# Performance work log

Measured on AMD Instinct MI355X. Metric: run time of the kernel, lower is better.

The kernel has to match this reference:

```python
import jax, jax.numpy as jnp
import numpy as np

BILATERAL = True
THETA_ALPHA = 8.0   # spatial bandwidth for bilateral term
THETA_BETA = 0.5    # color bandwidth for bilateral term
THETA_GAMMA = 3.0   # spatial bandwidth for spatial-only term


def _features(input_image):
    # input_image: [B, Ci, H, W] -> features [B, N, D]
    B, Ci, H, W = input_image.shape
    N = H * W
    ys, xs = jnp.meshgrid(jnp.arange(H, dtype=jnp.float32),
                          jnp.arange(W, dtype=jnp.float32), indexing='ij')
    pos = jnp.stack([ys, xs], axis=-1).reshape(N, 2)  # [N, 2]
    if BILATERAL:
        sp = jnp.broadcast_to(pos / THETA_ALPHA, (B, N, 2))
        col = input_image.reshape(B, Ci, N).transpose(0, 2, 1) / THETA_BETA  # [B, N, Ci]
        return jnp.concatenate([sp, col], axis=-1)  # [B, N, 2+Ci]
    else:
        return jnp.broadcast_to(pos / THETA_GAMMA, (B, N, 2))


def _gauss_filter(values, feats):
    # values: [B, C, N]; feats: [B, N, D] -> [B, C, N]
    # K_ij = exp(-0.5 * ||f_i - f_j||^2) (unnormalized, as in permutohedral filtering)
    sq = jnp.sum(feats * feats, axis=-1)  # [B, N]
    # squared distances: [B, N, N]
    d2 = sq[:, :, None] + sq[:, None, :] - 2.0 * jnp.einsum('bnd,bmd->bnm', feats, feats)
    K = jnp.exp(-0.5 * jnp.maximum(d2, 0.0))
    return jnp.einsum('bnm,bcm->bcn', K, values)


def setup_inputs() -> dict:
    key = jax.random.key(0)
    k1, k2 = jax.random.split(key)
    cur_state = jax.random.normal(k1, (2, 21, 96, 96), dtype=jnp.float32)
    input_image = jax.random.uniform(k2, (2, 3, 96, 96), dtype=jnp.float32)
    return {"cur_state": cur_state, "input_image": input_image}


def reference(cur_state, input_image):
    assert cur_state.ndim == 4
    B, C, H, W = cur_state.shape
    N = H * W
    feats = _features(input_image)                 # [B, N, D]
    vals = cur_state.reshape(B, C, N)              # [B, C, N]
    out = _gauss_filter(vals, feats)               # [B, C, N]
    return out.reshape(B, C, H, W)
```

## Files before the change

kernel.cpp:

```cpp
#include <hip/hip_runtime.h>
#include <hip/hip_bf16.h>
#include <math.h>


#define HH 96
#define WW 96
#define NN (HH * WW)
#define NB 2
#define NC 21

typedef __attribute__((ext_vector_type(8))) short short8;
typedef __attribute__((ext_vector_type(16))) float f32x16;

constexpr float INV_TA = 0.125f;
constexpr float INV_TB = 2.0f;
constexpr float LOG2E  = 1.44269504088896340736f;

constexpr int BLK   = 256;
constexpr int ITILE = 128;
constexpr int NIT   = NN / ITILE;
constexpr int NJB   = NN / 32;
constexpr int G     = 24;
constexpr int QW    = NJB / G;

constexpr size_t VG_BYTES = (size_t)NB * NJB * 128 * 16;
constexpr size_t FJA_OFF  = VG_BYTES;

constexpr int NVU = NB * NJB * 128;
constexpr int NFT = NB * NN;
constexpr int NZ  = NB * NC * NN / 4;
constexpr int PREP_TASKS = NVU + NFT + NZ;

#if defined(__has_builtin)
#if __has_builtin(__builtin_amdgcn_exp2f)
#define EXP2F(x) __builtin_amdgcn_exp2f(x)
#endif
#endif
#ifndef EXP2F
#define EXP2F(x) exp2f(x)
#endif

__device__ __forceinline__ unsigned short bf16_rne(float f) {
    __hip_bfloat16 h = __float2bfloat16(f);
    unsigned short u; __builtin_memcpy(&u, &h, 2); return u;
}
__device__ __forceinline__ float bf16_f(unsigned short u) {
    __hip_bfloat16 h; __builtin_memcpy(&h, &u, 2); return __bfloat162float(h);
}
__device__ __forceinline__ unsigned pk2(float a, float b) {
    const unsigned u0 = __float_as_uint(a) + 0x8000u;
    const unsigned u1 = __float_as_uint(b) + 0x8000u;
    return __builtin_amdgcn_perm(u1, u0, 0x07060302u);
}

__global__ __launch_bounds__(BLK)
void prep_kernel(const float* __restrict__ cur, const float* __restrict__ img,
                 unsigned char* __restrict__ ws, float* __restrict__ out) {
    const int t = blockIdx.x * BLK + threadIdx.x;
    if (t < NVU) {
        const int c    = t & 31;
        const int h    = (t >> 5) & 1;
        const int m    = (t >> 6) & 1;
        const int jw   = t >> 7;
        const int b    = jw / NJB;
        const int jblk = jw % NJB;
        const int jb = jblk * 32 + m * 16 + 4 * h;
        float4 qa = {0, 0, 0, 0}, qb = {0, 0, 0, 0};
        if (c < NC) {
            const float* row = cur + ((size_t)b * NC + c) * NN;
            qa = *(const float4*)(row + jb);
            qb = *(const float4*)(row + jb + 8);
        }
        uint4 o;
        o.x = pk2(qa.x, qa.y); o.y = pk2(qa.z, qa.w);
        o.z = pk2(qb.x, qb.y); o.w = pk2(qb.z, qb.w);
        *(uint4*)(ws + (size_t)t * 16) = o;
    } else if (t < NVU + NFT) {
        const int tf = t - NVU;
        const int b = tf / NN;
        const int j = tf % NN;
        const float y = (float)(j / WW) * INV_TA;
        const float x = (float)(j % WW) * INV_TA;
        const float* ib = img + (size_t)b * 3 * NN;
        unsigned short ch[3], cl[3]; float cf[3];
        #pragma unroll
        for (int d = 0; d < 3; ++d) {
            const float c = ib[d * NN + j] * INV_TB;
            ch[d] = bf16_rne(c);
            const float chf = bf16_f(ch[d]);
            cl[d] = bf16_rne(c - chf);
            cf[d] = chf + bf16_f(cl[d]);
        }
        const float e = -0.5f * (y * y + x * x +
                                 cf[0] * cf[0] + cf[1] * cf[1] + cf[2] * cf[2]);
        const unsigned short eh = bf16_rne(e);
        const unsigned short el = bf16_rne(e - bf16_f(eh));
        const unsigned short yb = bf16_rne(y), xb = bf16_rne(x);
        const unsigned short one = 0x3F80;
        unsigned short* u0 = (unsigned short*)
            (ws + FJA_OFF + ((size_t)(b * 2 + 0) * NN + j) * 16);
        unsigned short* u1 = (unsigned short*)
            (ws + FJA_OFF + ((size_t)(b * 2 + 1) * NN + j) * 16);
        u0[0] = yb; u0[1] = xb; u0[2] = ch[0]; u0[3] = ch[1]; u0[4] = ch[2];
        u0[5] = cl[0]; u0[6] = cl[1]; u0[7] = cl[2];
        u1[0] = ch[0]; u1[1] = ch[1]; u1[2] = ch[2]; u1[3] = eh; u1[4] = el;
        u1[5] = one; u1[6] = one; u1[7] = 0;
    } else {
        ((float4*)out)[t - NVU - NFT] = float4{0.0f, 0.0f, 0.0f, 0.0f};
    }
}

__global__ __launch_bounds__(BLK)
void perm_gauss_mfma(const float* __restrict__ img,
                     const unsigned char* __restrict__ ws,
                     float* __restrict__ out) {
    __shared__ __align__(16) float tile[4 * 32 * 33];
    const int tid  = threadIdx.x;
    const int lane = tid & 63;
    const int wave = tid >> 6;
    const int il   = lane & 31;
    const int half = lane >> 5;

    const int it = blockIdx.x, g = blockIdx.y, b = blockIdx.z;
    const int ibase = it * ITILE + wave * 32;
    const float* imgb = img + (size_t)b * 3 * NN;
    float* outb = out + (size_t)b * NC * NN;

    const int ig = ibase + il;
    const float y = (float)(ig / WW) * INV_TA;
    const float x = (float)(ig % WW) * INV_TA;
    unsigned short ch[3], cl[3]; float cf[3];
    #pragma unroll
    for (int d = 0; d < 3; ++d) {
        const float c = imgb[d * NN + ig] * INV_TB;
        ch[d] = bf16_rne(c);
        const float chf = bf16_f(ch[d]);
        cl[d] = bf16_rne(c - chf);
        cf[d] = chf + bf16_f(cl[d]);
    }
    const float e = -0.5f * (y * y + x * x +
                             cf[0] * cf[0] + cf[1] * cf[1] + cf[2] * cf[2]);
    const unsigned short eh = bf16_rne(e);
    const unsigned short el = bf16_rne(e - bf16_f(eh));
    const unsigned short one = 0x3F80;
    union { unsigned short u[8]; short8 v; } bfi;
    if (half == 0) {
        bfi.u[0] = bf16_rne(y); bfi.u[1] = bf16_rne(x);
        bfi.u[2] = ch[0]; bfi.u[3] = ch[1]; bfi.u[4] = ch[2];
        bfi.u[5] = ch[0]; bfi.u[6] = ch[1]; bfi.u[7] = ch[2];
    } else {
        bfi.u[0] = cl[0]; bfi.u[1] = cl[1]; bfi.u[2] = cl[2];
        bfi.u[3] = one; bfi.u[4] = one; bfi.u[5] = eh; bfi.u[6] = el;
        bfi.u[7] = 0;
    }

    f32x16 acc, zz;
    #pragma unroll
    for (int r = 0; r < 16; ++r) { acc[r] = 0.0f; zz[r] = 0.0f; }

    const int jb0 = g * QW;
    const unsigned char* fp = ws + FJA_OFF +
        ((size_t)(b * 2 + half) * NN + (size_t)jb0 * 32 + il) * 16;
    const unsigned char* vp = ws +
        ((size_t)(b * NJB + jb0) * 128 + half * 32 + il) * 16;

    auto consume = [&](const f32x16& s, short8 V1, short8 V2) {
        float w[16];
        #pragma unroll
        for (int r = 0; r < 16; ++r) w[r] = EXP2F(s[r] * LOG2E);
        union { unsigned dw[4]; short8 v; } a1, a2;
        #pragma unroll
        for (int d = 0; d < 4; ++d) {
            a1.dw[d] = pk2(w[2 * d],     w[2 * d + 1]);
            a2.dw[d] = pk2(w[8 + 2 * d], w[9 + 2 * d]);
        }
        acc = __builtin_amdgcn_mfma_f32_32x32x16_bf16(a1.v, V1, acc, 0, 0, 0);
        acc = __builtin_amdgcn_mfma_f32_32x32x16_bf16(a2.v, V2, acc, 0, 0, 0);
    };

    short8 af0 = *(const short8*)fp;
    short8 af1 = *(const short8*)(fp + 512);
    short8 v1  = *(const short8*)vp;
    short8 v2  = *(const short8*)(vp + 1024);
    f32x16 s_cur = __builtin_amdgcn_mfma_f32_32x32x16_bf16(af0, bfi.v, zz, 0, 0, 0);

    #pragma unroll 2
    for (int q = 0; q < QW - 1; ++q) {
        const f32x16 s_next =
            __builtin_amdgcn_mfma_f32_32x32x16_bf16(af1, bfi.v, zz, 0, 0, 0);
        if (q < QW - 2) af1 = *(const short8*)(fp + 1024);
        fp += 512;
        const short8 v1n = *(const short8*)(vp + 2048);
        const short8 v2n = *(const short8*)(vp + 2048 + 1024);
        vp += 2048;
        consume(s_cur, v1, v2);
        s_cur = s_next; v1 = v1n; v2 = v2n;
    }
    consume(s_cur, v1, v2);

    float* mytile = tile + wave * (32 * 33);
    #pragma unroll
    for (int r = 0; r < 16; ++r) {
        const int row = (r & 3) + 8 * (r >> 2) + 4 * half;
        mytile[row * 33 + il] = acc[r];
    }
    #pragma unroll
    for (int cc = 0; cc < 11; ++cc) {
        const int c = 2 * cc + half;
        if (c < NC) {
            const float v = mytile[il * 33 + c];
            atomicAdd(&outb[(size_t)c * NN + ibase + il], v);
        }
    }
}

extern "C" void kernel_launch(void* const* d_in, const int* in_sizes, int n_in,
                              void* d_out, int out_size, void* d_ws, size_t ws_size,
                              hipStream_t stream) {
    const float* cur = (const float*)d_in[0];
    const float* img = (const float*)d_in[1];
    float* out = (float*)d_out;
    unsigned char* ws = (unsigned char*)d_ws;

    prep_kernel<<<PREP_TASKS / BLK, BLK, 0, stream>>>(cur, img, ws, out);
    dim3 grid(NIT, G, NB);
    perm_gauss_mfma<<<grid, BLK, 0, stream>>>(img, ws, out);
}
```

Baseline: 93.94 us.

## Split j-range across waves with in-block reduction before atomics

```diff
diff --git a/kernel.cpp b/kernel.cpp
--- a/kernel.cpp
+++ b/kernel.cpp
@@ -17,11 +17,11 @@
 constexpr float LOG2E  = 1.44269504088896340736f;
 
 constexpr int BLK   = 256;
-constexpr int ITILE = 128;
+constexpr int ITILE = 32;
 constexpr int NIT   = NN / ITILE;
 constexpr int NJB   = NN / 32;
-constexpr int G     = 24;
-constexpr int QW    = NJB / G;
+constexpr int G2    = 6;
+constexpr int QW    = NJB / (G2*4);
 
 constexpr size_t VG_BYTES = (size_t)NB * NJB * 128 * 16;
 constexpr size_t FJA_OFF  = VG_BYTES;
@@ -51,6 +51,10 @@
     const unsigned u0 = __float_as_uint(a) + 0x8000u;
     const unsigned u1 = __float_as_uint(b) + 0x8000u;
     return __builtin_amdgcn_perm(u1, u0, 0x07060302u);
+}
+__device__ __forceinline__ unsigned pkrn(float a, float b) {
+    __hip_bfloat162 h = __float22bfloat162_rn(float2{a, b});
+    unsigned u; __builtin_memcpy(&u, &h, 4); return u;
 }
 
 __global__ __launch_bounds__(BLK)
@@ -122,7 +126,7 @@
     const int half = lane >> 5;
 
     const int it = blockIdx.x, g = blockIdx.y, b = blockIdx.z;
-    const int ibase = it * ITILE + wave * 32;
+    const int ibase = it * ITILE;
     const float* imgb = img + (size_t)b * 3 * NN;
     float* outb = out + (size_t)b * NC * NN;
 
@@ -158,7 +162,7 @@
     #pragma unroll
     for (int r = 0; r < 16; ++r) { acc[r] = 0.0f; zz[r] = 0.0f; }
 
-    const int jb0 = g * QW;
+    const int jb0 = (g * 4 + wave) * QW;
     const unsigned char* fp = ws + FJA_OFF +
         ((size_t)(b * 2 + half) * NN + (size_t)jb0 * 32 + il) * 16;
     const unsigned char* vp = ws +
@@ -171,8 +175,8 @@
         union { unsigned dw[4]; short8 v; } a1, a2;
         #pragma unroll
         for (int d = 0; d < 4; ++d) {
-            a1.dw[d] = pk2(w[2 * d],     w[2 * d + 1]);
-            a2.dw[d] = pk2(w[8 + 2 * d], w[9 + 2 * d]);
+            a1.dw[d] = pkrn(w[2 * d],     w[2 * d + 1]);
+            a2.dw[d] = pkrn(w[8 + 2 * d], w[9 + 2 * d]);
         }
         acc = __builtin_amdgcn_mfma_f32_32x32x16_bf16(a1.v, V1, acc, 0, 0, 0);
         acc = __builtin_amdgcn_mfma_f32_32x32x16_bf16(a2.v, V2, acc, 0, 0, 0);
@@ -204,12 +208,18 @@
         const int row = (r & 3) + 8 * (r >> 2) + 4 * half;
         mytile[row * 33 + il] = acc[r];
     }
-    #pragma unroll
-    for (int cc = 0; cc < 11; ++cc) {
-        const int c = 2 * cc + half;
+    __syncthreads();
+    const int ci = tid >> 5;
+    const int ii = tid & 31;
+    #pragma unroll
+    for (int cc = 0; cc < 3; ++cc) {
+        const int c = cc * 8 + ci;
         if (c < NC) {
-            const float v = mytile[il * 33 + c];
-            atomicAdd(&outb[(size_t)c * NN + ibase + il], v);
+            const float v = tile[0 * 1056 + ii * 33 + c]
+                          + tile[1 * 1056 + ii * 33 + c]
+                          + tile[2 * 1056 + ii * 33 + c]
+                          + tile[3 * 1056 + ii * 33 + c];
+            atomicAdd(&outb[(size_t)c * NN + ibase + ii], v);
         }
     }
 }
@@ -223,6 +233,6 @@
     unsigned char* ws = (unsigned char*)d_ws;
 
     prep_kernel<<<PREP_TASKS / BLK, BLK, 0, stream>>>(cur, img, ws, out);
-    dim3 grid(NIT, G, NB);
+    dim3 grid(NIT, G2, NB);
     perm_gauss_mfma<<<grid, BLK, 0, stream>>>(img, ws, out);
 }
```

After: 91.98 us. 2.1% less time.
